# Optimization experiments

Measured on AMD Instinct MI355X. Metric: run time of the kernel, lower is better.

Reference implementation:

```python
import jax, jax.numpy as jnp
import numpy as np

NEG = -1000000.0

def setup_inputs() -> dict:
    key = jax.random.key(0)
    ks = jax.random.split(key, 7)
    B, Q, K, H, Dv = 8, 512, 512, 64, 64
    queries = jax.random.normal(ks[0], (B, Q, H), dtype=jnp.float32)
    keys = jax.random.normal(ks[1], (B, K, H), dtype=jnp.float32)
    values = jax.random.normal(ks[2], (B, K, Dv), dtype=jnp.float32)
    valid_lens = jax.random.randint(ks[3], (B,), 1, K + 1)
    # learned params (torch Linear without bias); stored as [in, out]
    Wq = jax.random.normal(ks[4], (H, H), dtype=jnp.float32) / np.sqrt(H)
    Wk = jax.random.normal(ks[5], (H, H), dtype=jnp.float32) / np.sqrt(H)
    wv = jax.random.normal(ks[6], (H,), dtype=jnp.float32) / np.sqrt(H)
    return {"queries": queries, "keys": keys, "values": values,
            "valid_lens": valid_lens, "Wq": Wq, "Wk": Wk, "wv": wv}

def reference(queries, keys, values, valid_lens, Wq, Wk, wv):
    q = queries @ Wq                      # [B,Q,H]
    k = keys @ Wk                         # [B,K,H]
    # broadcast-add -> tanh -> rank-1 score projection
    feat = jnp.tanh(q[:, :, None, :] + k[:, None, :, :])   # [B,Q,K,H]
    scores = jnp.einsum('bqkh,h->bqk', feat, wv)            # [B,Q,K]
    # masked softmax over key axis: positions >= valid_len get -1e6
    Klen = scores.shape[-1]
    mask = jnp.arange(Klen)[None, None, :] < valid_lens[:, None, None]
    scores = jnp.where(mask, scores, NEG)
    attn = jax.nn.softmax(scores, axis=-1)                  # [B,Q,K]
    return jnp.einsum('bqk,bkd->bqd', attn, values)         # [B,Q,Dv]
```

## Files before the change

### kernel.cpp

```cpp
#include <hip/hip_runtime.h>

#define C2   2.8853900817779268f
#define NC2 -2.8853900817779268f

__global__ __launch_bounds__(256) void proj_exp_kernel(
    const float* __restrict__ queries,
    const float* __restrict__ keys,
    const float* __restrict__ Wq,
    const float* __restrict__ Wk,
    float* __restrict__ Eq,
    float* __restrict__ Ek)
{
    __shared__ float w_lds[64 * 64];
    __shared__ float in_lds[256];

    const int t   = threadIdx.x;
    const int blk = blockIdx.x;
    const int r0  = blk * 4;
    const bool isQ = (r0 < 4096);
    const float* __restrict__ W  = isQ ? Wq : Wk;
    const float* __restrict__ in = isQ ? queries : keys;
    float* __restrict__ Eo       = isQ ? Eq : Ek;
    const int rbase = isQ ? r0 : (r0 - 4096);

#pragma unroll
    for (int i = 0; i < 16; ++i)
        w_lds[t + i * 256] = W[t + i * 256];
    in_lds[t] = in[(size_t)rbase * 64 + t];
    __syncthreads();

    const int h  = t & 63;
    const int rl = t >> 6;
    float acc = 0.f;
#pragma unroll
    for (int i = 0; i < 64; ++i)
        acc = fmaf(in_lds[rl * 64 + i], w_lds[i * 64 + h], acc);

    float x = fminf(fmaxf(acc * C2, -60.f), 60.f);
    Eo[(size_t)rbase * 64 + t] = __builtin_amdgcn_exp2f(x);
}

__global__ __launch_bounds__(512, 4) void attn_kernel(
    const float* __restrict__ Eq,
    const float* __restrict__ Ek,
    const float* __restrict__ wv,
    const float* __restrict__ V,
    const int* __restrict__ valid_lens,
    float* __restrict__ out)
{
    __shared__ float p_lds[8][512];
    __shared__ float part_lds[8 * 8 * 64];
    __shared__ float wsum[8][8];

    const int t   = threadIdx.x;
    const int bid = blockIdx.x;
    const int b   = bid >> 6;
    const int q0  = (bid & 63) << 3;
    const int l   = t & 63;
    const int w   = __builtin_amdgcn_readfirstlane(threadIdx.x >> 6);
    const int vl  = valid_lens[b];
    const int k   = w * 64 + l;
    const bool kvalid = (k < vl);

    float ek[64];
    {
        const float4* ekr = reinterpret_cast<const float4*>(Ek + (size_t)(b * 512 + k) * 64);
#pragma unroll
        for (int i = 0; i < 16; ++i) {
            float4 v = ekr[i];
            ek[4 * i + 0] = v.x; ek[4 * i + 1] = v.y;
            ek[4 * i + 2] = v.z; ek[4 * i + 3] = v.w;
        }
    }

    const float* __restrict__ eqbase = Eq + (size_t)(b * 512 + q0) * 64;

#pragma unroll 1
    for (int q = 0; q < 8; ++q) {
        const float* __restrict__ eqp = eqbase + q * 64;
        float a0 = 0.f, a1 = 0.f;
#pragma unroll
        for (int h = 0; h < 64; h += 2) {
            a0 = fmaf(wv[h + 0], __builtin_amdgcn_rcpf(fmaf(eqp[h + 0], ek[h + 0], 1.f)), a0);
            a1 = fmaf(wv[h + 1], __builtin_amdgcn_rcpf(fmaf(eqp[h + 1], ek[h + 1], 1.f)), a1);
        }
        float p = kvalid ? __builtin_amdgcn_exp2f((a0 + a1) * NC2) : 0.f;
        p_lds[q][k] = p;
        float ps = p;
#pragma unroll
        for (int off = 32; off > 0; off >>= 1) ps += __shfl_xor(ps, off);
        if (l == 0) wsum[w][q] = ps;
    }

    const float* __restrict__ Vb = V + (size_t)b * 512 * 64;
    float acc[8] = {0.f, 0.f, 0.f, 0.f, 0.f, 0.f, 0.f, 0.f};
    const int kb = w * 64;
#pragma unroll 4
    for (int kk = 0; kk < 64; kk += 4) {
        const int k0 = kb + kk;
        float4 pq[8];
#pragma unroll
        for (int q = 0; q < 8; ++q)
            pq[q] = *reinterpret_cast<const float4*>(&p_lds[q][k0]);
        float v0 = Vb[(size_t)(k0 + 0) * 64 + l];
        float v1 = Vb[(size_t)(k0 + 1) * 64 + l];
        float v2 = Vb[(size_t)(k0 + 2) * 64 + l];
        float v3 = Vb[(size_t)(k0 + 3) * 64 + l];
#pragma unroll
        for (int q = 0; q < 8; ++q) {
            acc[q] = fmaf(pq[q].x, v0, acc[q]);
            acc[q] = fmaf(pq[q].y, v1, acc[q]);
            acc[q] = fmaf(pq[q].z, v2, acc[q]);
            acc[q] = fmaf(pq[q].w, v3, acc[q]);
        }
    }
#pragma unroll
    for (int q = 0; q < 8; ++q)
        part_lds[(w * 8 + q) * 64 + l] = acc[q];
    __syncthreads();

    float denom = 0.f, o = 0.f;
#pragma unroll
    for (int ww = 0; ww < 8; ++ww) {
        denom += wsum[ww][w];
        o     += part_lds[(ww * 8 + w) * 64 + l];
    }
    out[(size_t)(b * 512 + q0 + w) * 64 + l] = o * __builtin_amdgcn_rcpf(denom);
}

extern "C" void kernel_launch(void* const* d_in, const int* in_sizes, int n_in,
                              void* d_out, int out_size, void* d_ws, size_t ws_size,
                              hipStream_t stream) {
    (void)in_sizes; (void)n_in; (void)out_size; (void)ws_size;
    const float* queries = (const float*)d_in[0];
    const float* keys    = (const float*)d_in[1];
    const float* values  = (const float*)d_in[2];
    const int*   vlens   = (const int*)d_in[3];
    const float* Wq      = (const float*)d_in[4];
    const float* Wk      = (const float*)d_in[5];
    const float* wv      = (const float*)d_in[6];
    float* out = (float*)d_out;

    float* Eq = (float*)d_ws;
    float* Ek = Eq + 8 * 512 * 64;

    proj_exp_kernel<<<2048, 256, 0, stream>>>(queries, keys, Wq, Wk, Eq, Ek);
    attn_kernel<<<512, 512, 0, stream>>>(Eq, Ek, wv, values, vlens, out);
}
```

Baseline: 37.20 us.

## Process 16 rows per projection block and compute softmax denominator after barrier

The projection kernel now handles 16 rows per block instead of 4, with each thread computing 4 rows at once. This reuses each W value loaded from LDS and cuts the number of blocks that each reload the 16KB weight matrix. The attention kernel drops the per-query wave shuffle reduction in the score loop and instead sums the denominator from p_lds after the barrier. It also splits the score dot product into four accumulators for more instruction-level parallelism. The trade-off is fewer projection blocks (less parallelism) and slightly more LDS reads at the end.

New measurement: 39.02 us. +4.9%, slower.

```diff
diff --git a/kernel.cpp b/kernel.cpp
--- a/kernel.cpp
+++ b/kernel.cpp
@@ -12,11 +12,11 @@
     float* __restrict__ Ek)
 {
     __shared__ float w_lds[64 * 64];
-    __shared__ float in_lds[256];
+    __shared__ float in_lds[16 * 64];
 
     const int t   = threadIdx.x;
     const int blk = blockIdx.x;
-    const int r0  = blk * 4;
+    const int r0  = blk * 16;
     const bool isQ = (r0 < 4096);
     const float* __restrict__ W  = isQ ? Wq : Wk;
     const float* __restrict__ in = isQ ? queries : keys;
@@ -26,18 +26,40 @@
 #pragma unroll
     for (int i = 0; i < 16; ++i)
         w_lds[t + i * 256] = W[t + i * 256];
-    in_lds[t] = in[(size_t)rbase * 64 + t];
+#pragma unroll
+    for (int i = 0; i < 4; ++i)
+        in_lds[t + i * 256] = in[(size_t)rbase * 64 + t + i * 256];
     __syncthreads();
 
     const int h  = t & 63;
-    const int rl = t >> 6;
-    float acc = 0.f;
+    const int rg = t >> 6;
+    const float* inr = &in_lds[rg * 4 * 64];
+    float acc0 = 0.f, acc1 = 0.f, acc2 = 0.f, acc3 = 0.f;
 #pragma unroll
-    for (int i = 0; i < 64; ++i)
-        acc = fmaf(in_lds[rl * 64 + i], w_lds[i * 64 + h], acc);
-
-    float x = fminf(fmaxf(acc * C2, -60.f), 60.f);
-    Eo[(size_t)rbase * 64 + t] = __builtin_amdgcn_exp2f(x);
+    for (int i = 0; i < 64; i += 4) {
+        float4 r0_ = *reinterpret_cast<const float4*>(inr + 0 * 64 + i);
+        float4 r1_ = *reinterpret_cast<const float4*>(inr + 1 * 64 + i);
+        float4 r2_ = *reinterpret_cast<const float4*>(inr + 2 * 64 + i);
+        float4 r3_ = *reinterpret_cast<const float4*>(inr + 3 * 64 + i);
+        float w0 = w_lds[(i + 0) * 64 + h];
+        float w1 = w_lds[(i + 1) * 64 + h];
+        float w2 = w_lds[(i + 2) * 64 + h];
+        float w3 = w_lds[(i + 3) * 64 + h];
+        acc0 = fmaf(r0_.x, w0, acc0); acc0 = fmaf(r0_.y, w1, acc0);
+        acc0 = fmaf(r0_.z, w2, acc0); acc0 = fmaf(r0_.w, w3, acc0);
+        acc1 = fmaf(r1_.x, w0, acc1); acc1 = fmaf(r1_.y, w1, acc1);
+        acc1 = fmaf(r1_.z, w2, acc1); acc1 = fmaf(r1_.w, w3, acc1);
+        acc2 = fmaf(r2_.x, w0, acc2); acc2 = fmaf(r2_.y, w1, acc2);
+        acc2 = fmaf(r2_.z, w2, acc2); acc2 = fmaf(r2_.w, w3, acc2);
+        acc3 = fmaf(r3_.x, w0, acc3); acc3 = fmaf(r3_.y, w1, acc3);
+        acc3 = fmaf(r3_.z, w2, acc3); acc3 = fmaf(r3_.w, w3, acc3);
+    }
+    float a[4] = {acc0, acc1, acc2, acc3};
+#pragma unroll
+    for (int j = 0; j < 4; ++j) {
+        float x = fminf(fmaxf(a[j] * C2, -60.f), 60.f);
+        Eo[(size_t)(rbase + rg * 4 + j) * 64 + h] = __builtin_amdgcn_exp2f(x);
+    }
 }
 
 __global__ __launch_bounds__(512, 4) void attn_kernel(
@@ -50,7 +72,6 @@
 {
     __shared__ float p_lds[8][512];
     __shared__ float part_lds[8 * 8 * 64];
-    __shared__ float wsum[8][8];
 
     const int t   = threadIdx.x;
     const int bid = blockIdx.x;
@@ -78,18 +99,16 @@
 #pragma unroll 1
     for (int q = 0; q < 8; ++q) {
         const float* __restrict__ eqp = eqbase + q * 64;
-        float a0 = 0.f, a1 = 0.f;
+        float a0 = 0.f, a1 = 0.f, a2 = 0.f, a3 = 0.f;
 #pragma unroll
-        for (int h = 0; h < 64; h += 2) {
+        for (int h = 0; h < 64; h += 4) {
             a0 = fmaf(wv[h + 0], __builtin_amdgcn_rcpf(fmaf(eqp[h + 0], ek[h + 0], 1.f)), a0);
             a1 = fmaf(wv[h + 1], __builtin_amdgcn_rcpf(fmaf(eqp[h + 1], ek[h + 1], 1.f)), a1);
+            a2 = fmaf(wv[h + 2], __builtin_amdgcn_rcpf(fmaf(eqp[h + 2], ek[h + 2], 1.f)), a2);
+            a3 = fmaf(wv[h + 3], __builtin_amdgcn_rcpf(fmaf(eqp[h + 3], ek[h + 3], 1.f)), a3);
         }
-        float p = kvalid ? __builtin_amdgcn_exp2f((a0 + a1) * NC2) : 0.f;
+        float p = kvalid ? __builtin_amdgcn_exp2f(((a0 + a1) + (a2 + a3)) * NC2) : 0.f;
         p_lds[q][k] = p;
-        float ps = p;
-#pragma unroll
-        for (int off = 32; off > 0; off >>= 1) ps += __shfl_xor(ps, off);
-        if (l == 0) wsum[w][q] = ps;
     }
 
     const float* __restrict__ Vb = V + (size_t)b * 512 * 64;
@@ -119,13 +138,19 @@
         part_lds[(w * 8 + q) * 64 + l] = acc[q];
     __syncthreads();
 
-    float denom = 0.f, o = 0.f;
+    float dsum = 0.f;
 #pragma unroll
-    for (int ww = 0; ww < 8; ++ww) {
-        denom += wsum[ww][w];
-        o     += part_lds[(ww * 8 + w) * 64 + l];
-    }
-    out[(size_t)(b * 512 + q0 + w) * 64 + l] = o * __builtin_amdgcn_rcpf(denom);
+    for (int j = 0; j < 8; ++j)
+        dsum += p_lds[w][j * 64 + l];
+#pragma unroll
+    for (int off = 32; off > 0; off >>= 1)
+        dsum += __shfl_xor(dsum, off);
+
+    float o = 0.f;
+#pragma unroll
+    for (int ww = 0; ww < 8; ++ww)
+        o += part_lds[(ww * 8 + w) * 64 + l];
+    out[(size_t)(b * 512 + q0 + w) * 64 + l] = o * __builtin_amdgcn_rcpf(dsum);
 }
 
 extern "C" void kernel_launch(void* const* d_in, const int* in_sizes, int n_in,
@@ -144,6 +169,6 @@
     float* Eq = (float*)d_ws;
     float* Ek = Eq + 8 * 512 * 64;
 
-    proj_exp_kernel<<<2048, 256, 0, stream>>>(queries, keys, Wq, Wk, Eq, Ek);
+    proj_exp_kernel<<<512, 256, 0, stream>>>(queries, keys, Wq, Wk, Eq, Ek);
     attn_kernel<<<512, 512, 0, stream>>>(Eq, Ek, wv, values, vlens, out);
 }
```
